# Kernel optimization log

Measured on AMD Instinct MI355X. Metric: run time of the kernel, lower is better.

Reference implementation:

```python
import jax, jax.numpy as jnp
import numpy as np

MIN_NORM = 1e-15
BALL_EPS = 1e-5  # proj margin, c = 1
HYPER_BETA = 1.0


def _artanh(x):
    x = jnp.clip(x, -1.0 + 1e-7, 1.0 - 1e-7)
    return jnp.arctanh(x)


def _proj(x):
    # clip points inside the unit Poincare ball
    norm = jnp.maximum(jnp.linalg.norm(x, axis=-1, keepdims=True), MIN_NORM)
    maxnorm = 1.0 - BALL_EPS
    return jnp.where(norm > maxnorm, x / norm * maxnorm, x)


def _expmap0(u):
    un = jnp.maximum(jnp.linalg.norm(u, axis=-1, keepdims=True), MIN_NORM)
    return jnp.tanh(un) * u / un


def _mobius_add(x, y):
    x2 = jnp.sum(x * x, axis=-1, keepdims=True)
    y2 = jnp.sum(y * y, axis=-1, keepdims=True)
    xy = jnp.sum(x * y, axis=-1, keepdims=True)
    num = (1.0 + 2.0 * xy + y2) * x + (1.0 - x2) * y
    den = 1.0 + 2.0 * xy + x2 * y2
    return num / jnp.maximum(den, MIN_NORM)


def _sqdist(p, q):
    ma = _mobius_add(-p, q)
    d = 2.0 * _artanh(jnp.linalg.norm(ma, axis=-1))
    return d * d


def _to_klein(x):
    return 2.0 * x / (1.0 + jnp.sum(x * x, axis=-1, keepdims=True))


def _lorentz_factor(x):
    return 1.0 / jnp.sqrt(jnp.maximum(1.0 - jnp.sum(x * x, axis=-1), 1e-7))


def _klein_to(x):
    return x / (1.0 + jnp.sqrt(jnp.maximum(1.0 - jnp.sum(x * x, axis=-1, keepdims=True), 0.0)))


def _logmap0(p):
    pn = jnp.maximum(jnp.linalg.norm(p, axis=-1, keepdims=True), MIN_NORM)
    return _artanh(pn) * p / pn


def setup_inputs() -> dict:
    key = jax.random.key(0)
    k1, k2, k3, k4, k5 = jax.random.split(key, 5)
    B, L, V, D, A, S = 4096, 50, 50000, 200, 14, 30
    inputs = jax.random.randint(k1, (B, L), 0, V, dtype=jnp.int32)
    emb = jax.random.normal(k2, (V, D), dtype=jnp.float32) * 0.1  # w2v * 0.1 as in student_init
    xav = float(np.sqrt(6.0 / (D + D)))
    M = jax.random.uniform(k3, (D, D), dtype=jnp.float32, minval=-xav, maxval=xav)
    a_emb = jax.random.normal(k4, (A, S, D), dtype=jnp.float32) * 0.1
    sw = jax.random.uniform(k5, (A, S), dtype=jnp.float32)
    seed_w = sw / jnp.sum(jnp.abs(sw), axis=1, keepdims=True)  # L1-normalized
    return {"inputs": inputs, "emb": emb, "M": M, "a_emb": a_emb, "seed_w": seed_w}


def reference(inputs, emb, M, a_emb, seed_w):
    # --- AttentionEncoder ---
    x_wrd = emb[inputs]                                   # [B,L,D] gather
    x_avg = jnp.mean(x_wrd, axis=1)                       # [B,D]
    scores = jnp.einsum('bld,de,be->bl', x_wrd, M, x_avg)  # [B,L]
    a = jax.nn.softmax(scores, axis=1)
    enc = jnp.einsum('bl,bld->bd', a, x_wrd)              # [B,D]

    # --- hyperbolic projection ---
    enc = _proj(_expmap0(enc))                            # [B,D] on Poincare ball
    a_emb_w = jnp.sum(a_emb * seed_w[:, :, None], axis=1)  # [A,D]
    hyp_a = _proj(_expmap0(a_emb_w))                      # [A,D]

    sqd = _sqdist(enc[:, None, :], hyp_a[None, :, :])     # [B,A]
    probs_exp = jnp.exp(-HYPER_BETA * sqd - 0.05)         # [B,A]
    a_probs = probs_exp / jnp.sum(probs_exp, axis=1, keepdims=True)

    kle = _to_klein(hyp_a)                                # [A,D]
    lf = _lorentz_factor(kle)                             # [A]
    probs = lf[None, :] * probs_exp                       # [B,A]
    probs_expanded = (probs / jnp.sum(probs, axis=1, keepdims=True))[:, :, None]  # [B,A,1]

    kle_o = jnp.sum(kle[None, :, :] * probs_expanded, axis=1)  # [B,D] Klein barycenter
    r = _klein_to(kle_o)                                  # [B,D]
    eu_r = _logmap0(r)                                    # [B,D]
    return eu_r, probs_expanded, a_probs
```

## Files before the change

kernel.cpp:

```cpp
#include <hip/hip_runtime.h>
#include <hip/hip_fp16.h>
#include <math.h>

#define B_ 4096
#define L_ 50
#define D_ 200
#define A_ 14
#define S_ 30

#define WS_HYP   0
#define WS_KLE   (A_ * D_)
#define WS_Y2    (2 * A_ * D_)
#define WS_LF    (WS_Y2 + A_)
#define WS_MH    8192
#define WS_V     8192

__device__ __forceinline__ float wave_reduce_sum(float v) {
    #pragma unroll
    for (int off = 32; off > 0; off >>= 1) v += __shfl_down(v, off, 64);
    return v;
}
__device__ __forceinline__ float bfly_sum(float v) {
    #pragma unroll
    for (int m = 32; m > 0; m >>= 1) v += __shfl_xor(v, m, 64);
    return v;
}
__device__ __forceinline__ float bfly_sum16(float v) {
    #pragma unroll
    for (int m = 8; m > 0; m >>= 1) v += __shfl_xor(v, m, 64);
    return v;
}
__device__ __forceinline__ float block_reduce_512(float val, volatile float* red) {
    __syncthreads();
    val = wave_reduce_sum(val);
    if ((threadIdx.x & 63) == 0) red[threadIdx.x >> 6] = val;
    __syncthreads();
    float s = 0.f;
    #pragma unroll
    for (int i = 0; i < 8; ++i) s += red[i];
    return s;
}

typedef _Float16 h2v __attribute__((ext_vector_type(2)));
__device__ __forceinline__ float fd2(unsigned a, unsigned b, float c) {
#if __has_builtin(__builtin_amdgcn_fdot2)
    return __builtin_amdgcn_fdot2(__builtin_bit_cast(h2v, a),
                                  __builtin_bit_cast(h2v, b), c, false);
#else
    __half2 ha = __builtin_bit_cast(__half2, a), hb = __builtin_bit_cast(__half2, b);
    float2 fa = __half22float2(ha), fb = __half22float2(hb);
    return fmaf(fa.x, fb.x, fmaf(fa.y, fb.y, c));
#endif
}
__device__ __forceinline__ unsigned packh2(float a, float b) {
    __half2 h = __floats2half2_rn(a, b);
    return __builtin_bit_cast(unsigned, h);
}

__global__ __launch_bounds__(256) void precompute_anchors(
    const float* __restrict__ a_emb, const float* __restrict__ seed_w,
    float* __restrict__ ws)
{
    __shared__ float u[A_][D_];
    __shared__ float nrm2[A_];
    const int t = threadIdx.x;
    const int wave = t >> 6, lane = t & 63;

    for (int d = t; d < D_; d += 256) {
        for (int a = 0; a < A_; ++a) {
            float acc = 0.f;
            #pragma unroll 5
            for (int s = 0; s < S_; ++s)
                acc += a_emb[(a * S_ + s) * D_ + d] * seed_w[a * S_ + s];
            u[a][d] = acc;
        }
    }
    __syncthreads();

    for (int a = wave; a < A_; a += 4) {
        float s = 0.f;
        for (int d = lane; d < D_; d += 64) s += u[a][d] * u[a][d];
        s = wave_reduce_sum(s);
        if (lane == 0) nrm2[a] = s;
    }
    __syncthreads();

    float* hyp = ws + WS_HYP;
    float* kle = ws + WS_KLE;
    float* y2  = ws + WS_Y2;
    float* lf  = ws + WS_LF;
    const float maxn = 1.0f - 1e-5f;

    for (int a = 0; a < A_; ++a) {
        float un = fmaxf(sqrtf(nrm2[a]), 1e-15f);
        float th = tanhf(un);
        float pn = fminf(th, maxn);
        float s  = pn / un;
        float py2 = pn * pn;
        float kscale = 2.0f / (1.0f + py2);
        float k2 = py2 * kscale * kscale;
        if (t == 0) {
            y2[a] = py2;
            lf[a] = 1.0f / sqrtf(fmaxf(1.0f - k2, 1e-7f));
        }
        for (int d = t; d < D_; d += 256) {
            float h = u[a][d] * s;
            hyp[a * D_ + d] = h;
            kle[a * D_ + d] = h * kscale;
        }
    }
}

__global__ __launch_bounds__(256) void convert_M(
    const float* __restrict__ M, __half* __restrict__ Mh)
{
    int i = blockIdx.x * 256 + threadIdx.x;
    if (i < D_ * D_) Mh[i] = __float2half(M[i]);
}

__global__ __launch_bounds__(256, 4) void fused_wave(
    const int*   __restrict__ inputs,
    const float* __restrict__ emb,
    const float* __restrict__ ws,
    float* __restrict__ out)
{
    const float*  kle = ws + WS_KLE;
    const float*  y2  = ws + WS_Y2;
    const float*  lf  = ws + WS_LF;
    const __half* Mh  = (const __half*)(ws + WS_MH);

    const int wid  = threadIdx.x >> 6, lane = threadIdx.x & 63;
    const int b    = blockIdx.x * 4 + wid;
    const bool L50 = (lane < 50);

    const int sidx = inputs[b * L_ + (L50 ? lane : 0)];
    const int off  = L50 ? 4 * lane : 0;

    float a0 = 0.f, a1 = 0.f, a2 = 0.f, a3 = 0.f;
    {
        #pragma unroll 10
        for (int l = 0; l < L_; ++l) {
            const int row = __shfl(sidx, l, 64);
            float4 x = *(const float4*)(emb + (size_t)row * D_ + off);
            a0 += x.x; a1 += x.y; a2 += x.z; a3 += x.w;
        }
    }
    const float inv = 1.0f / (float)L_;
    unsigned xu0 = packh2(a0 * inv, a1 * inv);
    unsigned xu1 = packh2(a2 * inv, a3 * inv);

    float v0 = 0.f, v1 = 0.f, v2 = 0.f, v3 = 0.f;
    {
        const int mr = L50 ? 4 * lane : 0;
        const __half* m0 = Mh + (size_t)(mr + 0) * D_;
        const __half* m1 = Mh + (size_t)(mr + 1) * D_;
        const __half* m2 = Mh + (size_t)(mr + 2) * D_;
        const __half* m3 = Mh + (size_t)(mr + 3) * D_;
        #pragma unroll 5
        for (int c = 0; c < 25; ++c) {
            unsigned xa = __shfl(xu0, 2 * c,     64);
            unsigned xb = __shfl(xu1, 2 * c,     64);
            unsigned xc = __shfl(xu0, 2 * c + 1, 64);
            unsigned xd = __shfl(xu1, 2 * c + 1, 64);
            uint4 q0 = *(const uint4*)(m0 + 8 * c);
            uint4 q1 = *(const uint4*)(m1 + 8 * c);
            uint4 q2 = *(const uint4*)(m2 + 8 * c);
            uint4 q3 = *(const uint4*)(m3 + 8 * c);
            v0 = fd2(q0.x, xa, v0); v0 = fd2(q0.y, xb, v0); v0 = fd2(q0.z, xc, v0); v0 = fd2(q0.w, xd, v0);
            v1 = fd2(q1.x, xa, v1); v1 = fd2(q1.y, xb, v1); v1 = fd2(q1.z, xc, v1); v1 = fd2(q1.w, xd, v1);
            v2 = fd2(q2.x, xa, v2); v2 = fd2(q2.y, xb, v2); v2 = fd2(q2.z, xc, v2); v2 = fd2(q2.w, xd, v2);
            v3 = fd2(q3.x, xa, v3); v3 = fd2(q3.y, xb, v3); v3 = fd2(q3.z, xc, v3); v3 = fd2(q3.w, xd, v3);
        }
    }

    float m = -INFINITY, ssum = 0.f;
    float e0 = 0.f, e1 = 0.f, e2 = 0.f, e3 = 0.f;
    {
        float4 bufA[10], bufB[10];

        auto LOADC = [&](float4* xb, int base) {
            #pragma unroll
            for (int j = 0; j < 10; ++j) {
                const int r = __shfl(sidx, base + j, 64);
                xb[j] = *(const float4*)(emb + (size_t)r * D_ + off);
            }
        };
        auto PROC = [&](const float4* xb) {
            #pragma unroll
            for (int j = 0; j < 10; ++j) {
                const float4 x = xb[j];
                float part = L50 ? (x.x * v0 + x.y * v1 + x.z * v2 + x.w * v3) : 0.f;
                const float s = bfly_sum(part);
                if (s > m) {
                    const float r = expf(m - s);
                    ssum *= r; e0 *= r; e1 *= r; e2 *= r; e3 *= r;
                    m = s;
                }
                const float w = expf(s - m);
                ssum += w;
                e0 = fmaf(w, x.x, e0); e1 = fmaf(w, x.y, e1);
                e2 = fmaf(w, x.z, e2); e3 = fmaf(w, x.w, e3);
            }
        };

        LOADC(bufA, 0);
        LOADC(bufB, 10); PROC(bufA);
        LOADC(bufA, 20); PROC(bufB);
        LOADC(bufB, 30); PROC(bufA);
        LOADC(bufA, 40); PROC(bufB);
        PROC(bufA);

        const float rs = 1.0f / ssum;
        e0 *= rs; e1 *= rs; e2 *= rs; e3 *= rs;
        if (!L50) { e0 = e1 = e2 = e3 = 0.f; }
    }

    const float n2 = bfly_sum(e0 * e0 + e1 * e1 + e2 * e2 + e3 * e3);
    const float un = fmaxf(sqrtf(n2), 1e-15f);
    const float pn = fminf(tanhf(un), 1.0f - 1e-5f);
    const float ps = pn / un;
    const float x2 = pn * pn;
    const float p0 = e0 * ps, p1 = e1 * ps, p2 = e2 * ps, p3 = e3 * ps;

    const int koff = off;
    float kd = 0.f;
    #pragma unroll
    for (int a = 0; a < A_; ++a) {
        float4 k = *(const float4*)(kle + a * D_ + koff);
        float part = L50 ? (p0 * k.x + p1 * k.y + p2 * k.z + p3 * k.w) : 0.f;
        float d = bfly_sum(part);
        if (lane == a) kd = d;
    }

    float px = 0.f, lfv = 0.f;
    if (lane < A_) {
        const float yy  = y2[lane];
        lfv = lf[lane];
        const float dot = kd * (1.0f + yy) * 0.5f;
        const float c1 = 1.0f - 2.0f * dot + yy;
        const float c2 = 1.0f - x2;
        const float num2 = c1 * c1 * x2 - 2.0f * c1 * c2 * dot + c2 * c2 * yy;
        const float den  = fmaxf(1.0f - 2.0f * dot + x2 * yy, 1e-15f);
        const float nma  = sqrtf(fmaxf(num2, 0.f)) / den;
        const float z    = fminf(nma, 1.0f - 1e-7f);
        const float dist = logf((1.0f + z) / (1.0f - z));
        px = expf(-dist * dist - 0.05f);
    }
    const float se = bfly_sum16(px);
    const float sp = bfly_sum16(lfv * px);
    float pev = 0.f;
    if (lane < A_) {
        pev = lfv * px / sp;
        out[B_ * D_ + b * A_ + lane] = pev;
        out[B_ * D_ + B_ * A_ + b * A_ + lane] = px / se;
    }

    float k0 = 0.f, k1 = 0.f, k2 = 0.f, k3 = 0.f;
    #pragma unroll
    for (int a = 0; a < A_; ++a) {
        const float w = __shfl(pev, a, 64);
        float4 k = *(const float4*)(kle + a * D_ + koff);
        k0 = fmaf(w, k.x, k0); k1 = fmaf(w, k.y, k1);
        k2 = fmaf(w, k.z, k2); k3 = fmaf(w, k.w, k3);
    }
    if (!L50) { k0 = k1 = k2 = k3 = 0.f; }
    const float n2k = bfly_sum(k0 * k0 + k1 * k1 + k2 * k2 + k3 * k3);
    const float denom = 1.0f + sqrtf(fmaxf(1.0f - n2k, 0.f));
    const float r2 = n2k / (denom * denom);
    const float rn = fmaxf(sqrtf(r2), 1e-15f);
    const float z2 = fminf(rn, 1.0f - 1e-7f);
    const float fac = 0.5f * logf((1.0f + z2) / (1.0f - z2)) / rn;
    if (L50) {
        float4 o = make_float4(fac * k0 / denom, fac * k1 / denom,
                               fac * k2 / denom, fac * k3 / denom);
        *(float4*)(out + (size_t)b * D_ + 4 * lane) = o;
    }
}

#define G_R 8
__global__ __launch_bounds__(512) void gather_gemm(
    const int* __restrict__ inputs, const float* __restrict__ emb,
    const float* __restrict__ M, float* __restrict__ ws)
{
    __shared__ __align__(16) float xs[G_R][D_ + 4];
    __shared__ int sidx[G_R][L_];
    float* v = ws + WS_V;
    const int b0 = blockIdx.x * G_R;
    const int t = threadIdx.x;
    const int wave = t >> 6, lane = t & 63;

    for (int p = t; p < G_R * L_; p += 512) sidx[p / L_][p % L_] = inputs[b0 * L_ + p];
    __syncthreads();

    if (lane < D_ / 4) {
        float ax = 0.f, ay = 0.f, az = 0.f, aw = 0.f;
        #pragma unroll
        for (int l = 0; l < L_; ++l) {
            const float4 vv = ((const float4*)(emb + (size_t)sidx[wave][l] * D_))[lane];
            ax += vv.x; ay += vv.y; az += vv.z; aw += vv.w;
        }
        const float inv = 1.0f / (float)L_;
        ((float4*)xs[wave])[lane] = make_float4(ax * inv, ay * inv, az * inv, aw * inv);
    }
    __syncthreads();

    const int r = t & 7, dg = t >> 3;
    const float4* xr4 = (const float4*)xs[r];
    #pragma unroll
    for (int k = 0; k < 4; ++k) {
        const int d = dg + 64 * k;
        if (d < D_) {
            const float4* Mr4 = (const float4*)(M + d * D_);
            float acc = 0.f;
            #pragma unroll
            for (int e = 0; e < D_ / 4; ++e) {
                float4 m4 = Mr4[e], x4 = xr4[e];
                acc += m4.x * x4.x + m4.y * x4.y + m4.z * x4.z + m4.w * x4.w;
            }
            v[(size_t)(b0 + r) * D_ + d] = acc;
        }
    }
}

__global__ __launch_bounds__(512, 8) void fused_main(
    const int*   __restrict__ inputs,
    const float* __restrict__ emb,
    const float* __restrict__ ws,
    float* __restrict__ out)
{
    __shared__ __align__(16) float x[L_][D_];
    __shared__ float attn[L_];
    __shared__ int   sidx[L_];
    __shared__ float red[8];
    __shared__ float sums[2];

    const float* hyp = ws + WS_HYP;
    const float* kle = ws + WS_KLE;
    const float* y2  = ws + WS_Y2;
    const float* lf  = ws + WS_LF;
    const float* vg  = ws + WS_V;

    const int b = blockIdx.x;
    const int t = threadIdx.x;
    const int wave = t >> 6, lane = t & 63;

    float vr0 = vg[(size_t)b * D_ + lane];
    float vr1 = vg[(size_t)b * D_ + lane + 64];
    float vr2 = vg[(size_t)b * D_ + lane + 128];
    float vr3 = (lane < D_ - 192) ? vg[(size_t)b * D_ + lane + 192] : 0.f;

    if (t < L_) sidx[t] = inputs[b * L_ + t];
    __syncthreads();

    {
        const int DQ = D_ / 4;
        const int p0 = t, p1 = t + 512, p2 = t + 1024, p3 = t + 1536, p4 = t + 2048;
        const bool has4 = (p4 < L_ * DQ);
        float4 a0 = ((const float4*)(emb + (size_t)sidx[p0 / DQ] * D_))[p0 % DQ];
        float4 a1 = ((const float4*)(emb + (size_t)sidx[p1 / DQ] * D_))[p1 % DQ];
        float4 a2 = ((const float4*)(emb + (size_t)sidx[p2 / DQ] * D_))[p2 % DQ];
        float4 a3 = ((const float4*)(emb + (size_t)sidx[p3 / DQ] * D_))[p3 % DQ];
        float4 a4;
        if (has4) a4 = ((const float4*)(emb + (size_t)sidx[p4 / DQ] * D_))[p4 % DQ];
        ((float4*)x[p0 / DQ])[p0 % DQ] = a0;
        ((float4*)x[p1 / DQ])[p1 % DQ] = a1;
        ((float4*)x[p2 / DQ])[p2 % DQ] = a2;
        ((float4*)x[p3 / DQ])[p3 % DQ] = a3;
        if (has4) ((float4*)x[p4 / DQ])[p4 % DQ] = a4;
    }
    __syncthreads();

    for (int l = wave; l < L_; l += 8) {
        float s = x[l][lane] * vr0 + x[l][lane + 64] * vr1 + x[l][lane + 128] * vr2;
        if (lane < D_ - 192) s += x[l][lane + 192] * vr3;
        s = wave_reduce_sum(s);
        if (lane == 0) attn[l] = s;
    }
    __syncthreads();

    if (wave == 0) {
        float scv = (lane < L_) ? attn[lane] : -INFINITY;
        float m = scv;
        #pragma unroll
        for (int off = 32; off > 0; off >>= 1) m = fmaxf(m, __shfl_xor(m, off, 64));
        float e = (lane < L_) ? expf(scv - m) : 0.f;
        float ss = e;
        #pragma unroll
        for (int off = 32; off > 0; off >>= 1) ss += __shfl_xor(ss, off, 64);
        if (lane < L_) attn[lane] = e / ss;
    }
    __syncthreads();

    float encv = 0.f;
    if (t < D_) {
        #pragma unroll 10
        for (int l = 0; l < L_; ++l) encv += attn[l] * x[l][t];
    }

    float n2 = block_reduce_512((t < D_) ? encv * encv : 0.f, red);
    const float maxn = 1.0f - 1e-5f;
    float un = fmaxf(sqrtf(n2), 1e-15f);
    float pn = fminf(tanhf(un), maxn);
    float ps = pn / un;
    float x2 = pn * pn;
    float* pvec  = &x[0][0];
    float* dotpq = &x[1][0];
    float* pexp  = &x[1][16];
    float* pe    = &x[1][32];
    if (t < D_) pvec[t] = encv * ps;
    __syncthreads();

    for (int a = wave; a < A_; a += 8) {
        const float* ha = hyp + a * D_;
        float s = ha[lane] * pvec[lane] + ha[lane + 64] * pvec[lane + 64]
                + ha[lane + 128] * pvec[lane + 128];
        if (lane < D_ - 192) s += ha[lane + 192] * pvec[lane + 192];
        s = wave_reduce_sum(s);
        if (lane == 0) dotpq[a] = s;
    }
    __syncthreads();

    if (t < A_) {
        float dot = dotpq[t];
        float yy  = y2[t];
        float c1 = 1.0f - 2.0f * dot + yy;
        float c2 = 1.0f - x2;
        float num2 = c1 * c1 * x2 - 2.0f * c1 * c2 * dot + c2 * c2 * yy;
        float den  = fmaxf(1.0f - 2.0f * dot + x2 * yy, 1e-15f);
        float nma  = sqrtf(fmaxf(num2, 0.f)) / den;
        float z    = fminf(nma, 1.0f - 1e-7f);
        float dist = logf((1.0f + z) / (1.0f - z));
        pexp[t] = expf(-dist * dist - 0.05f);
    }
    __syncthreads();
    if (t == 0) {
        float se = 0.f, sp = 0.f;
        for (int a = 0; a < A_; ++a) { se += pexp[a]; sp += lf[a] * pexp[a]; }
        sums[0] = 1.0f / se;
        sums[1] = 1.0f / sp;
    }
    __syncthreads();
    if (t < A_) {
        float ap  = pexp[t] * sums[0];
        float pev = lf[t] * pexp[t] * sums[1];
        pe[t] = pev;
        out[B_ * D_ + b * A_ + t] = pev;
        out[B_ * D_ + B_ * A_ + b * A_ + t] = ap;
    }
    __syncthreads();

    float ko = 0.f;
    if (t < D_) {
        #pragma unroll
        for (int a = 0; a < A_; ++a) ko += kle[a * D_ + t] * pe[a];
    }
    float n2k = block_reduce_512((t < D_) ? ko * ko : 0.f, red);
    if (t < D_) {
        float denom = 1.0f + sqrtf(fmaxf(1.0f - n2k, 0.f));
        float rv = ko / denom;
        float r2 = n2k / (denom * denom);
        float rn = fmaxf(sqrtf(r2), 1e-15f);
        float z  = fminf(rn, 1.0f - 1e-7f);
        float fac = (0.5f * logf((1.0f + z) / (1.0f - z))) / rn;
        out[b * D_ + t] = fac * rv;
    }
}

extern "C" void kernel_launch(void* const* d_in, const int* in_sizes, int n_in,
                              void* d_out, int out_size, void* d_ws, size_t ws_size,
                              hipStream_t stream) {
    (void)in_sizes; (void)n_in; (void)out_size;
    const int*   inputs = (const int*)  d_in[0];
    const float* emb    = (const float*)d_in[1];
    const float* M      = (const float*)d_in[2];
    const float* a_emb  = (const float*)d_in[3];
    const float* seed_w = (const float*)d_in[4];
    float* out = (float*)d_out;
    float* ws  = (float*)d_ws;

    precompute_anchors<<<1, 256, 0, stream>>>(a_emb, seed_w, ws);

    const size_t need = (size_t)(WS_MH + (D_ * D_ + 1) / 2) * sizeof(float);
    if (ws_size >= need) {
        __half* Mh = (__half*)(ws + WS_MH);
        convert_M<<<(D_ * D_ + 255) / 256, 256, 0, stream>>>(M, Mh);
        fused_wave<<<B_ / 4, 256, 0, stream>>>(inputs, emb, ws, out);
    } else {
        gather_gemm<<<B_ / G_R, 512, 0, stream>>>(inputs, emb, M, ws);
        fused_main<<<B_, 512, 0, stream>>>(inputs, emb, ws, out);
    }
}
```

Baseline: 117.9 us.

## Split each batch row across two waves with LDS-merged online softmax

Each batch row is now processed by two wavefronts instead of one. Each wave gathers half of the 50 tokens, and each computes half of the M·x_avg matvec. Partial sums, the matvec outputs and the online-softmax state (max, sum, weighted accumulators) are exchanged through shared memory and merged with three block barriers. The goal is to double wave-level parallelism and shorten each wave's serial gather/softmax chain, at the cost of barriers, LDS traffic and the tail hyperbolic math being computed redundantly by both waves.

```diff
diff --git a/kernel.cpp b/kernel.cpp
--- a/kernel.cpp
+++ b/kernel.cpp
@@ -118,44 +118,62 @@
     if (i < D_ * D_) Mh[i] = __float2half(M[i]);
 }
 
-__global__ __launch_bounds__(256, 4) void fused_wave(
+__global__ __launch_bounds__(256, 6) void fused_wave2(
     const int*   __restrict__ inputs,
     const float* __restrict__ emb,
     const float* __restrict__ ws,
     float* __restrict__ out)
 {
+    __shared__ float xav[2][2][D_];
+    __shared__ float vsh[2][D_];
+    __shared__ float ench[2][2][D_];
+    __shared__ float msh[2][2][2];
+
     const float*  kle = ws + WS_KLE;
     const float*  y2  = ws + WS_Y2;
     const float*  lf  = ws + WS_LF;
     const __half* Mh  = (const __half*)(ws + WS_MH);
 
     const int wid  = threadIdx.x >> 6, lane = threadIdx.x & 63;
-    const int b    = blockIdx.x * 4 + wid;
+    const int rib  = wid >> 1;
+    const int h    = wid & 1;
+    const int b    = blockIdx.x * 2 + rib;
     const bool L50 = (lane < 50);
 
     const int sidx = inputs[b * L_ + (L50 ? lane : 0)];
     const int off  = L50 ? 4 * lane : 0;
+    const int lbase = 25 * h;
 
     float a0 = 0.f, a1 = 0.f, a2 = 0.f, a3 = 0.f;
+    #pragma unroll 5
+    for (int j = 0; j < 25; ++j) {
+        const int row = __shfl(sidx, lbase + j, 64);
+        float4 x = *(const float4*)(emb + (size_t)row * D_ + off);
+        a0 += x.x; a1 += x.y; a2 += x.z; a3 += x.w;
+    }
+    if (L50) {
+        xav[rib][h][4 * lane + 0] = a0;
+        xav[rib][h][4 * lane + 1] = a1;
+        xav[rib][h][4 * lane + 2] = a2;
+        xav[rib][h][4 * lane + 3] = a3;
+    }
+    __syncthreads();
+    unsigned xu0 = 0, xu1 = 0;
+    if (L50) {
+        const float inv = 1.0f / (float)L_;
+        float f0 = (xav[rib][0][4 * lane + 0] + xav[rib][1][4 * lane + 0]) * inv;
+        float f1 = (xav[rib][0][4 * lane + 1] + xav[rib][1][4 * lane + 1]) * inv;
+        float f2 = (xav[rib][0][4 * lane + 2] + xav[rib][1][4 * lane + 2]) * inv;
+        float f3 = (xav[rib][0][4 * lane + 3] + xav[rib][1][4 * lane + 3]) * inv;
+        xu0 = packh2(f0, f1);
+        xu1 = packh2(f2, f3);
+    }
+
     {
-        #pragma unroll 10
-        for (int l = 0; l < L_; ++l) {
-            const int row = __shfl(sidx, l, 64);
-            float4 x = *(const float4*)(emb + (size_t)row * D_ + off);
-            a0 += x.x; a1 += x.y; a2 += x.z; a3 += x.w;
-        }
-    }
-    const float inv = 1.0f / (float)L_;
-    unsigned xu0 = packh2(a0 * inv, a1 * inv);
-    unsigned xu1 = packh2(a2 * inv, a3 * inv);
-
-    float v0 = 0.f, v1 = 0.f, v2 = 0.f, v3 = 0.f;
-    {
-        const int mr = L50 ? 4 * lane : 0;
+        float w0 = 0.f, w1 = 0.f;
+        const int mr = 100 * h + 2 * (L50 ? lane : 0);
         const __half* m0 = Mh + (size_t)(mr + 0) * D_;
         const __half* m1 = Mh + (size_t)(mr + 1) * D_;
-        const __half* m2 = Mh + (size_t)(mr + 2) * D_;
-        const __half* m3 = Mh + (size_t)(mr + 3) * D_;
         #pragma unroll 5
         for (int c = 0; c < 25; ++c) {
             unsigned xa = __shfl(xu0, 2 * c,     64);
@@ -164,30 +182,34 @@
             unsigned xd = __shfl(xu1, 2 * c + 1, 64);
             uint4 q0 = *(const uint4*)(m0 + 8 * c);
             uint4 q1 = *(const uint4*)(m1 + 8 * c);
-            uint4 q2 = *(const uint4*)(m2 + 8 * c);
-            uint4 q3 = *(const uint4*)(m3 + 8 * c);
-            v0 = fd2(q0.x, xa, v0); v0 = fd2(q0.y, xb, v0); v0 = fd2(q0.z, xc, v0); v0 = fd2(q0.w, xd, v0);
-            v1 = fd2(q1.x, xa, v1); v1 = fd2(q1.y, xb, v1); v1 = fd2(q1.z, xc, v1); v1 = fd2(q1.w, xd, v1);
-            v2 = fd2(q2.x, xa, v2); v2 = fd2(q2.y, xb, v2); v2 = fd2(q2.z, xc, v2); v2 = fd2(q2.w, xd, v2);
-            v3 = fd2(q3.x, xa, v3); v3 = fd2(q3.y, xb, v3); v3 = fd2(q3.z, xc, v3); v3 = fd2(q3.w, xd, v3);
-        }
+            w0 = fd2(q0.x, xa, w0); w0 = fd2(q0.y, xb, w0); w0 = fd2(q0.z, xc, w0); w0 = fd2(q0.w, xd, w0);
+            w1 = fd2(q1.x, xa, w1); w1 = fd2(q1.y, xb, w1); w1 = fd2(q1.z, xc, w1); w1 = fd2(q1.w, xd, w1);
+        }
+        if (L50) { vsh[rib][mr] = w0; vsh[rib][mr + 1] = w1; }
+    }
+    __syncthreads();
+    float v0 = 0.f, v1 = 0.f, v2 = 0.f, v3 = 0.f;
+    if (L50) {
+        v0 = vsh[rib][4 * lane + 0];
+        v1 = vsh[rib][4 * lane + 1];
+        v2 = vsh[rib][4 * lane + 2];
+        v3 = vsh[rib][4 * lane + 3];
     }
 
     float m = -INFINITY, ssum = 0.f;
     float e0 = 0.f, e1 = 0.f, e2 = 0.f, e3 = 0.f;
     {
-        float4 bufA[10], bufB[10];
-
+        float4 bufA[5], bufB[5];
         auto LOADC = [&](float4* xb, int base) {
             #pragma unroll
-            for (int j = 0; j < 10; ++j) {
-                const int r = __shfl(sidx, base + j, 64);
+            for (int j = 0; j < 5; ++j) {
+                const int r = __shfl(sidx, lbase + base + j, 64);
                 xb[j] = *(const float4*)(emb + (size_t)r * D_ + off);
             }
         };
         auto PROC = [&](const float4* xb) {
             #pragma unroll
-            for (int j = 0; j < 10; ++j) {
+            for (int j = 0; j < 5; ++j) {
                 const float4 x = xb[j];
                 float part = L50 ? (x.x * v0 + x.y * v1 + x.z * v2 + x.w * v3) : 0.f;
                 const float s = bfly_sum(part);
@@ -202,17 +224,38 @@
                 e2 = fmaf(w, x.z, e2); e3 = fmaf(w, x.w, e3);
             }
         };
-
         LOADC(bufA, 0);
-        LOADC(bufB, 10); PROC(bufA);
+        LOADC(bufB, 5);  PROC(bufA);
+        LOADC(bufA, 10); PROC(bufB);
+        LOADC(bufB, 15); PROC(bufA);
         LOADC(bufA, 20); PROC(bufB);
-        LOADC(bufB, 30); PROC(bufA);
-        LOADC(bufA, 40); PROC(bufB);
         PROC(bufA);
-
-        const float rs = 1.0f / ssum;
-        e0 *= rs; e1 *= rs; e2 *= rs; e3 *= rs;
-        if (!L50) { e0 = e1 = e2 = e3 = 0.f; }
+    }
+    if (L50) {
+        ench[rib][h][4 * lane + 0] = e0;
+        ench[rib][h][4 * lane + 1] = e1;
+        ench[rib][h][4 * lane + 2] = e2;
+        ench[rib][h][4 * lane + 3] = e3;
+    }
+    if (lane == 0) { msh[rib][h][0] = m; msh[rib][h][1] = ssum; }
+    __syncthreads();
+
+    {
+        const float mo  = msh[rib][1 - h][0];
+        const float sso = msh[rib][1 - h][1];
+        const float M   = fmaxf(m, mo);
+        const float wA  = expf(m - M);
+        const float wB  = expf(mo - M);
+        const float st  = ssum * wA + sso * wB;
+        const float rs  = 1.0f / st;
+        if (L50) {
+            e0 = (e0 * wA + ench[rib][1 - h][4 * lane + 0] * wB) * rs;
+            e1 = (e1 * wA + ench[rib][1 - h][4 * lane + 1] * wB) * rs;
+            e2 = (e2 * wA + ench[rib][1 - h][4 * lane + 2] * wB) * rs;
+            e3 = (e3 * wA + ench[rib][1 - h][4 * lane + 3] * wB) * rs;
+        } else {
+            e0 = e1 = e2 = e3 = 0.f;
+        }
     }
 
     const float n2 = bfly_sum(e0 * e0 + e1 * e1 + e2 * e2 + e3 * e3);
@@ -222,11 +265,10 @@
     const float x2 = pn * pn;
     const float p0 = e0 * ps, p1 = e1 * ps, p2 = e2 * ps, p3 = e3 * ps;
 
-    const int koff = off;
     float kd = 0.f;
     #pragma unroll
     for (int a = 0; a < A_; ++a) {
-        float4 k = *(const float4*)(kle + a * D_ + koff);
+        float4 k = *(const float4*)(kle + a * D_ + off);
         float part = L50 ? (p0 * k.x + p1 * k.y + p2 * k.z + p3 * k.w) : 0.f;
         float d = bfly_sum(part);
         if (lane == a) kd = d;
@@ -251,15 +293,17 @@
     float pev = 0.f;
     if (lane < A_) {
         pev = lfv * px / sp;
-        out[B_ * D_ + b * A_ + lane] = pev;
-        out[B_ * D_ + B_ * A_ + b * A_ + lane] = px / se;
+        if (h == 0) {
+            out[B_ * D_ + b * A_ + lane] = pev;
+            out[B_ * D_ + B_ * A_ + b * A_ + lane] = px / se;
+        }
     }
 
     float k0 = 0.f, k1 = 0.f, k2 = 0.f, k3 = 0.f;
     #pragma unroll
     for (int a = 0; a < A_; ++a) {
         const float w = __shfl(pev, a, 64);
-        float4 k = *(const float4*)(kle + a * D_ + koff);
+        float4 k = *(const float4*)(kle + a * D_ + off);
         k0 = fmaf(w, k.x, k0); k1 = fmaf(w, k.y, k1);
         k2 = fmaf(w, k.z, k2); k3 = fmaf(w, k.w, k3);
     }
@@ -270,7 +314,7 @@
     const float rn = fmaxf(sqrtf(r2), 1e-15f);
     const float z2 = fminf(rn, 1.0f - 1e-7f);
     const float fac = 0.5f * logf((1.0f + z2) / (1.0f - z2)) / rn;
-    if (L50) {
+    if (L50 && h == 0) {
         float4 o = make_float4(fac * k0 / denom, fac * k1 / denom,
                                fac * k2 / denom, fac * k3 / denom);
         *(float4*)(out + (size_t)b * D_ + 4 * lane) = o;
@@ -484,7 +528,7 @@
     if (ws_size >= need) {
         __half* Mh = (__half*)(ws + WS_MH);
         convert_M<<<(D_ * D_ + 255) / 256, 256, 0, stream>>>(M, Mh);
-        fused_wave<<<B_ / 4, 256, 0, stream>>>(inputs, emb, ws, out);
+        fused_wave2<<<B_ / 2, 256, 0, stream>>>(inputs, emb, ws, out);
     } else {
         gather_gemm<<<B_ / G_R, 512, 0, stream>>>(inputs, emb, M, ws);
         fused_main<<<B_, 512, 0, stream>>>(inputs, emb, ws, out);
```

New measurement: 111.2 us. -5.7%, faster.
